# Optimization experiments

Hardware: AMD Instinct MI355X
Metric: run time of the kernel (lower is better)

The kernel has to match this reference:

```python
import jax, jax.numpy as jnp
import numpy as np
from jax import lax

BZ, CAPACITY, SEQ_LEN, IN_VAR, N_EDGES = 64, 134, 288, 16, 96


def setup_inputs() -> dict:
    key = jax.random.key(0)
    ks = jax.random.split(key, 9)
    s_gcn = 1.0 / np.sqrt(SEQ_LEN)
    s_conv = 1.0 / np.sqrt(IN_VAR * 3)
    s_fc = 1.0 / np.sqrt(2 * IN_VAR)
    return {
        "src": jax.random.normal(ks[0], (BZ, CAPACITY, SEQ_LEN, IN_VAR), dtype=jnp.float32),
        "feature_edge_index": jax.random.randint(ks[1], (2, N_EDGES), 0, IN_VAR, dtype=jnp.int32),
        # SAGEConv(seq_len, seq_len): out = lin_l(mean_neighbors) + lin_r(x); lin_l has bias
        "Wl": jax.random.uniform(ks[2], (SEQ_LEN, SEQ_LEN), jnp.float32, -s_gcn, s_gcn),
        "Wr": jax.random.uniform(ks[3], (SEQ_LEN, SEQ_LEN), jnp.float32, -s_gcn, s_gcn),
        "b_gcn": jax.random.uniform(ks[4], (SEQ_LEN,), jnp.float32, -s_gcn, s_gcn),
        "conv1_w": jax.random.uniform(ks[5], (IN_VAR, IN_VAR, 3), jnp.float32, -s_conv, s_conv),
        "conv2_w": jax.random.uniform(ks[6], (IN_VAR, IN_VAR, 5), jnp.float32, -s_conv, s_conv),
        "fc_w": jax.random.uniform(ks[7], (IN_VAR, 2 * IN_VAR), jnp.float32, -s_fc, s_fc),
        "fc_b": jax.random.uniform(ks[8], (IN_VAR,), jnp.float32, -s_fc, s_fc),
    }


def reference(src, feature_edge_index, Wl, Wr, b_gcn, conv1_w, conv2_w, fc_w, fc_b):
    bz, cap, S, F = src.shape  # [bz, capacity, seq_len, in_var]
    B = bz * cap
    # node features for the feature graph: [B, in_var, seq_len]
    x2 = src.transpose(0, 1, 3, 2).reshape(B, F, S)
    e_src, e_dst = feature_edge_index[0], feature_edge_index[1]
    # SAGEConv mean aggregation over shared edge_index, vectorized across B graphs
    gathered = x2[:, e_src, :]                                   # [B, E, S]
    agg = jnp.zeros_like(x2).at[:, e_dst, :].add(gathered)       # [B, F, S]
    deg = jnp.zeros((F,), x2.dtype).at[e_dst].add(1.0)
    mean = agg / jnp.maximum(deg, 1.0)[None, :, None]
    feat = (jnp.einsum('bns,ts->bnt', mean, Wl)
            + jnp.einsum('bns,ts->bnt', x2, Wr) + b_gcn)          # [B, F, S]
    fea_fea = feat.reshape(bz, cap, F, S).transpose(0, 1, 3, 2)   # [bz,cap,S,F]
    # dual temporal Conv1d branches (same padding, no bias) on [B, F, S]
    dn = ('NCH', 'OIH', 'NCH')
    c1 = lax.conv_general_dilated(x2, conv1_w, (1,), [(1, 1)], dimension_numbers=dn)
    c2 = lax.conv_general_dilated(x2, conv2_w, (2,), [(2, 2)][:1] * 1, dimension_numbers=dn) if False else lax.conv_general_dilated(x2, conv2_w, (1,), [(2, 2)], dimension_numbers=dn)
    temporal = (c1 + c2).transpose(0, 2, 1).reshape(bz, cap, S, F)
    com = jnp.concatenate([fea_fea, temporal], axis=-1)           # [bz,cap,S,2F]
    com = jnp.einsum('bcsf,of->bcso', com, fc_w) + fc_b
    # dropout is identity in eval mode
    return src + com
```

## Files before the change

kernel.cpp:

```cpp
#include <hip/hip_runtime.h>
#include <hip/hip_bf16.h>

typedef short short8 __attribute__((ext_vector_type(8)));
typedef float float4v __attribute__((ext_vector_type(4)));
typedef unsigned short ushort4v __attribute__((ext_vector_type(4)));

#define BTOT 8576
#define SEQ 288
#define NF 16
#define SPN 296
#define XTROWS 294
#define XT_USH (XTROWS * 16)
#define XN_USH (16 * SPN)
#define PBN (XT_USH + XN_USH)
#define WCVW 104

__device__ __forceinline__ unsigned short f2b(float f) {
    union { float f; unsigned u; } v; v.f = f;
    unsigned r = v.u + 0x7FFF + ((v.u >> 16) & 1);
    return (unsigned short)(r >> 16);
}
__device__ __forceinline__ float b2f(unsigned short u) {
    union { unsigned u; float f; } v; v.u = ((unsigned)u) << 16; return v.f;
}

__global__ void wcast_kernel(const float* __restrict__ a, const float* __restrict__ b,
                             unsigned short* __restrict__ o) {
    int i = blockIdx.x * 256 + threadIdx.x;
    o[i]         = f2b(a[i]);
    o[82944 + i] = f2b(b[i]);
}

template<int WPRE>
__device__ __forceinline__ short8 ldw(const unsigned short* __restrict__ wb,
                                      const float* __restrict__ wf, int idx) {
    if (WPRE) {
        return *(const short8*)&wb[idx];
    } else {
        const float* p = &wf[idx];
        float4 w0 = *(const float4*)p, w1 = *(const float4*)(p + 4);
        short8 a;
        a[0] = (short)f2b(w0.x); a[1] = (short)f2b(w0.y);
        a[2] = (short)f2b(w0.z); a[3] = (short)f2b(w0.w);
        a[4] = (short)f2b(w1.x); a[5] = (short)f2b(w1.y);
        a[6] = (short)f2b(w1.z); a[7] = (short)f2b(w1.w);
        return a;
    }
}

#define LDB(KK9, B_) do {                                                      \
    const int s0_ = (KK9) * 32;                                                \
    (B_)[0] = *(const short8*)&xsN0[li * SPN + s0_ + 8 * g];                   \
    (B_)[1] = *(const short8*)&xsN1[li * SPN + s0_ + 8 * g];                   \
} while (0)

#define LDA(WT_, WF_, KK9, A_) do {                                            \
    const int s0_ = (KK9) * 32;                                                \
    _Pragma("unroll")                                                          \
    for (int m_ = 0; m_ < 3; ++m_)                                             \
        if (m_ < nt) (A_)[m_] = ldw<WPRE>(WT_, WF_, arow[m_] + s0_ + 8 * g);   \
} while (0)

#define MFK(A_, B_) do {                                                       \
    _Pragma("unroll")                                                          \
    for (int m_ = 0; m_ < 3; ++m_)                                             \
        if (m_ < nt) {                                                         \
            acc[m_][0] = __builtin_amdgcn_mfma_f32_16x16x32_bf16((A_)[m_], (B_)[0], acc[m_][0], 0, 0, 0); \
            acc[m_][1] = __builtin_amdgcn_mfma_f32_16x16x32_bf16((A_)[m_], (B_)[1], acc[m_][1], 0, 0, 0); \
        }                                                                      \
} while (0)

#define GEMM9(WT_, WF_) do {                                                   \
    short8 aC[3], aN[3];                                                       \
    LDA(WT_, WF_, 0, aC);                                                      \
    LDA(WT_, WF_, 1, aN);                                                      \
    _Pragma("unroll")                                                          \
    for (int kk = 0; kk < 9; ++kk) {                                           \
        short8 bb[2];                                                          \
        LDB(kk, bb);                                                           \
        if (kk & 1) { MFK(aN, bb); if (kk < 7) LDA(WT_, WF_, kk + 2, aN); }    \
        else        { MFK(aC, bb); if (kk < 7) LDA(WT_, WF_, kk + 2, aC); }    \
    }                                                                          \
} while (0)

template<int WPRE>
__global__ __launch_bounds__(512, 6) void stconv_mfma(
    const float* __restrict__ src,
    const int*   __restrict__ eidx,
    const float* __restrict__ Wlf,
    const float* __restrict__ Wrf,
    const unsigned short* __restrict__ Wbf,
    const float* __restrict__ bgcn,
    const float* __restrict__ cw1g,
    const float* __restrict__ cw2g,
    const float* __restrict__ fcwg,
    const float* __restrict__ fcbg,
    float*       __restrict__ out)
{
    __shared__ unsigned short pool[2 * PBN];
    __shared__ unsigned short wcv[16 * WCVW];
    __shared__ unsigned short fcwB[16 * 40];
    __shared__ unsigned short MB[16 * 40];
    __shared__ float bg[SEQ];
    __shared__ float Msc[256];
    __shared__ float fcb[16];

    const int tid  = threadIdx.x;
    const int wav  = tid >> 6;
    const int nb   = wav >> 2;
    const int wloc = wav & 3;
    const int lane = tid & 63;
    const int li   = lane & 15;
    const int g    = lane >> 4;
    const int b0   = blockIdx.x * 2;

    unsigned short* xsT = pool + nb * PBN;
    unsigned short* xsN = pool + nb * PBN + XT_USH;
    const float* srcb = src + (size_t)(b0 + nb) * (SEQ * NF);

    if (tid < 256) Msc[tid] = 0.0f;
    for (int i = tid; i < 16 * 40; i += 512) MB[i] = 0;
    for (int i = tid; i < 16 * WCVW; i += 512) wcv[i] = 0;
    if (tid < 192) {
        int nb2 = tid / 96, r2 = tid % 96;
        int r = r2 >> 4, f = r2 & 15;
        int row = (r < 2) ? r : 288 + r;
        pool[nb2 * PBN + row * 16 + f] = 0;
    }
    __syncthreads();

    if (tid < 96) atomicAdd(&Msc[eidx[96 + tid] * 16 + eidx[tid]], 1.0f);
    {
        const int q = tid & 255;
        #pragma unroll
        for (int i = 0; i < 2; ++i) {
            int blk = i * 256 + q;
            if (blk < 288) {
                int s0 = (blk >> 2) * 4, f0 = (blk & 3) * 4;
                ushort4v h[4];
                #pragma unroll
                for (int r = 0; r < 4; ++r) {
                    float4 v = *(const float4*)(srcb + (s0 + r) * 16 + f0);
                    h[r][0] = f2b(v.x); h[r][1] = f2b(v.y);
                    h[r][2] = f2b(v.z); h[r][3] = f2b(v.w);
                    *(ushort4v*)&xsT[(s0 + r + 2) * 16 + f0] = h[r];
                }
                #pragma unroll
                for (int c = 0; c < 4; ++c) {
                    ushort4v w;
                    w[0] = h[0][c]; w[1] = h[1][c]; w[2] = h[2][c]; w[3] = h[3][c];
                    *(ushort4v*)&xsN[(f0 + c) * SPN + s0] = w;
                }
            }
        }
    }
    for (int j = tid; j < 1280; j += 512) {
        int fo = j / 80, rem = j % 80, fi = rem / 5, d = rem % 5;
        float t = cw2g[(fo * 16 + fi) * 5 + d];
        if (d >= 1 && d <= 3) t += cw1g[(fo * 16 + fi) * 3 + (d - 1)];
        wcv[fo * WCVW + d * 16 + fi] = f2b(t);
    }
    if (tid < 512) fcwB[(tid >> 5) * 40 + (tid & 31)] = f2b(fcwg[tid]);
    if (tid < SEQ) bg[tid] = bgcn[tid];
    if (tid < 16) fcb[tid] = fcbg[tid];
    __syncthreads();

    if (tid < 16) {
        float deg = 0.0f;
        #pragma unroll
        for (int f = 0; f < 16; ++f) deg += Msc[tid * 16 + f];
        float inv = 1.0f / fmaxf(deg, 1.0f);
        #pragma unroll
        for (int f = 0; f < 16; ++f) MB[tid * 40 + f] = f2b(Msc[tid * 16 + f] * inv);
    }
    __syncthreads();

    const int t2 = (wav == 0) ? 16 : ((wav == 5) ? 17 : -1);
    const int nt = (t2 >= 0) ? 3 : 2;
    const int tts[3] = {wav, wav + 8, t2};
    const int arow[3] = {(tts[0] * 16 + li) * 288, (tts[1] * 16 + li) * 288,
                         (t2 >= 0) ? ((t2 * 16 + li) * 288) : 0};

    const unsigned short* WblT = Wbf;
    const unsigned short* WbrT = Wbf + 288 * 288;
    const unsigned short* xsN0 = pool + XT_USH;
    const unsigned short* xsN1 = pool + PBN + XT_USH;

    float4v acc[3][2];

    #pragma unroll
    for (int m = 0; m < 3; ++m)
        if (m < nt) {
            #pragma unroll
            for (int r = 0; r < 4; ++r) {
                float bv = bg[tts[m] * 16 + 4 * g + r];
                acc[m][0][r] = bv; acc[m][1][r] = bv;
            }
        }
    GEMM9(WbrT, Wrf);
    __syncthreads();

    {
        short8 bm = *(const short8*)&MB[li * 40 + 8 * g];
        unsigned short* msN = xsN;
        for (int st = wloc; st < 18; st += 4) {
            int s0 = st * 16;
            short8 a = {0, 0, 0, 0, 0, 0, 0, 0};
            if (g < 2) a = *(const short8*)&xsT[(s0 + li + 2) * 16 + 8 * g];
            float4v c = {0.f, 0.f, 0.f, 0.f};
            c = __builtin_amdgcn_mfma_f32_16x16x32_bf16(a, bm, c, 0, 0, 0);
            ushort4v p;
            #pragma unroll
            for (int r = 0; r < 4; ++r) p[r] = f2b(c[r]);
            *(ushort4v*)&msN[li * SPN + s0 + 4 * g] = p;
        }
    }
    __syncthreads();

    GEMM9(WblT, Wlf);

    ushort4v p5o[3][2];
    #pragma unroll
    for (int m = 0; m < 3; ++m)
        if (m < nt) {
            #pragma unroll
            for (int r = 0; r < 4; ++r) {
                p5o[m][0][r] = f2b(acc[m][0][r]);
                p5o[m][1][r] = f2b(acc[m][1][r]);
            }
        }

    ushort4v p6o[5];
    {
        short8 cb0 = *(const short8*)&wcv[li * WCVW + 0  + 8 * g];
        short8 cb1 = *(const short8*)&wcv[li * WCVW + 32 + 8 * g];
        short8 cb2 = *(const short8*)&wcv[li * WCVW + 64 + 8 * g];
        const int fi0   = (g & 1) * 8;
        const int dbase = g >> 1;
        #pragma unroll
        for (int it = 0; it < 5; ++it) {
            int st = wloc + 4 * it;
            if (st < 18) {
                int s0 = st * 16;
                int rbase = (s0 + li + dbase) * 16 + fi0;
                short8 a0 = *(const short8*)&xsT[rbase];
                short8 a1 = *(const short8*)&xsT[rbase + 32];
                short8 a2 = *(const short8*)&xsT[rbase + 64];
                float4v c = {0.f, 0.f, 0.f, 0.f};
                c = __builtin_amdgcn_mfma_f32_16x16x32_bf16(a0, cb0, c, 0, 0, 0);
                c = __builtin_amdgcn_mfma_f32_16x16x32_bf16(a1, cb1, c, 0, 0, 0);
                c = __builtin_amdgcn_mfma_f32_16x16x32_bf16(a2, cb2, c, 0, 0, 0);
                #pragma unroll
                for (int r = 0; r < 4; ++r) p6o[it][r] = f2b(c[r]);
            }
        }
    }

    ushort4v res16[5];
    #pragma unroll
    for (int it = 0; it < 5; ++it) {
        int st = wloc + 4 * it;
        if (st < 18) {
            int s0 = st * 16;
            #pragma unroll
            for (int r = 0; r < 4; ++r)
                res16[it][r] = xsT[(s0 + 4 * g + r + 2) * 16 + li];
        }
    }
    __syncthreads();

    {
        unsigned short* cat0 = pool;
        unsigned short* cat1 = pool + PBN;
        #pragma unroll
        for (int m = 0; m < 3; ++m)
            if (m < nt) {
                #pragma unroll
                for (int r = 0; r < 4; ++r) {
                    int pos = tts[m] * 16 + 4 * g + r;
                    cat0[pos * 32 + li] = p5o[m][0][r];
                    cat1[pos * 32 + li] = p5o[m][1][r];
                }
            }
        unsigned short* catb = pool + nb * PBN;
        #pragma unroll
        for (int it = 0; it < 5; ++it) {
            int st = wloc + 4 * it;
            if (st < 18) {
                int s0 = st * 16;
                #pragma unroll
                for (int r = 0; r < 4; ++r)
                    catb[(s0 + 4 * g + r) * 32 + 16 + li] = p6o[it][r];
            }
        }
    }
    __syncthreads();

    {
        const unsigned short* catb = pool + nb * PBN;
        short8 fb = *(const short8*)&fcwB[li * 40 + 8 * g];
        float* outb = out + (size_t)(b0 + nb) * (SEQ * NF);
        #pragma unroll
        for (int it = 0; it < 5; ++it) {
            int st = wloc + 4 * it;
            if (st < 18) {
                int s0 = st * 16;
                float4v c;
                #pragma unroll
                for (int r = 0; r < 4; ++r) c[r] = b2f(res16[it][r]) + fcb[li];
                short8 a = *(const short8*)&catb[(s0 + li) * 32 + 8 * g];
                c = __builtin_amdgcn_mfma_f32_16x16x32_bf16(a, fb, c, 0, 0, 0);
                #pragma unroll
                for (int r = 0; r < 4; ++r) outb[(s0 + 4 * g + r) * 16 + li] = c[r];
            }
        }
    }
}

extern "C" void kernel_launch(void* const* d_in, const int* in_sizes, int n_in,
                              void* d_out, int out_size, void* d_ws, size_t ws_size,
                              hipStream_t stream)
{
    const float* src  = (const float*)d_in[0];
    const int*   eidx = (const int*)  d_in[1];
    const float* Wl   = (const float*)d_in[2];
    const float* Wr   = (const float*)d_in[3];
    const float* bgcn = (const float*)d_in[4];
    const float* cw1  = (const float*)d_in[5];
    const float* cw2  = (const float*)d_in[6];
    const float* fcw  = (const float*)d_in[7];
    const float* fcb  = (const float*)d_in[8];
    float* out = (float*)d_out;

    const size_t wbytes = (size_t)2 * 288 * 288 * sizeof(unsigned short);
    if (ws_size >= wbytes) {
        wcast_kernel<<<dim3(324), dim3(256), 0, stream>>>(Wl, Wr, (unsigned short*)d_ws);
        stconv_mfma<1><<<dim3(BTOT / 2), dim3(512), 0, stream>>>(
            src, eidx, Wl, Wr, (const unsigned short*)d_ws,
            bgcn, cw1, cw2, fcw, fcb, out);
    } else {
        stconv_mfma<0><<<dim3(BTOT / 2), dim3(512), 0, stream>>>(
            src, eidx, Wl, Wr, nullptr,
            bgcn, cw1, cw2, fcw, fcb, out);
    }
}
```

Baseline: 157.8 us.

## Process one graph per 256-thread block instead of two per 512-thread block

Changes the work split so each block handles a single graph with 4 waves. Each wave now owns 4–5 output row tiles of the 288x288 GEMM instead of 2–3 tiles across two graphs. Per block, weight A-fragments are reused across more M-tiles rather than across two B operands. This halves LDS per block and may allow more resident blocks, but each weight load now feeds only one graph, roughly doubling global and L2 weight traffic per graph.

```diff
diff --git a/kernel.cpp b/kernel.cpp
--- a/kernel.cpp
+++ b/kernel.cpp
@@ -50,33 +50,30 @@
 
 #define LDB(KK9, B_) do {                                                      \
     const int s0_ = (KK9) * 32;                                                \
-    (B_)[0] = *(const short8*)&xsN0[li * SPN + s0_ + 8 * g];                   \
-    (B_)[1] = *(const short8*)&xsN1[li * SPN + s0_ + 8 * g];                   \
+    (B_) = *(const short8*)&xsN[li * SPN + s0_ + 8 * g];                       \
 } while (0)
 
 #define LDA(WT_, WF_, KK9, A_) do {                                            \
     const int s0_ = (KK9) * 32;                                                \
     _Pragma("unroll")                                                          \
-    for (int m_ = 0; m_ < 3; ++m_)                                             \
+    for (int m_ = 0; m_ < 5; ++m_)                                             \
         if (m_ < nt) (A_)[m_] = ldw<WPRE>(WT_, WF_, arow[m_] + s0_ + 8 * g);   \
 } while (0)
 
 #define MFK(A_, B_) do {                                                       \
     _Pragma("unroll")                                                          \
-    for (int m_ = 0; m_ < 3; ++m_)                                             \
-        if (m_ < nt) {                                                         \
-            acc[m_][0] = __builtin_amdgcn_mfma_f32_16x16x32_bf16((A_)[m_], (B_)[0], acc[m_][0], 0, 0, 0); \
-            acc[m_][1] = __builtin_amdgcn_mfma_f32_16x16x32_bf16((A_)[m_], (B_)[1], acc[m_][1], 0, 0, 0); \
-        }                                                                      \
+    for (int m_ = 0; m_ < 5; ++m_)                                             \
+        if (m_ < nt)                                                           \
+            acc[m_] = __builtin_amdgcn_mfma_f32_16x16x32_bf16((A_)[m_], (B_), acc[m_], 0, 0, 0); \
 } while (0)
 
 #define GEMM9(WT_, WF_) do {                                                   \
-    short8 aC[3], aN[3];                                                       \
+    short8 aC[5], aN[5];                                                       \
     LDA(WT_, WF_, 0, aC);                                                      \
     LDA(WT_, WF_, 1, aN);                                                      \
     _Pragma("unroll")                                                          \
     for (int kk = 0; kk < 9; ++kk) {                                           \
-        short8 bb[2];                                                          \
+        short8 bb;                                                             \
         LDB(kk, bb);                                                           \
         if (kk & 1) { MFK(aN, bb); if (kk < 7) LDA(WT_, WF_, kk + 2, aN); }    \
         else        { MFK(aC, bb); if (kk < 7) LDA(WT_, WF_, kk + 2, aC); }    \
@@ -84,7 +81,7 @@
 } while (0)
 
 template<int WPRE>
-__global__ __launch_bounds__(512, 6) void stconv_mfma(
+__global__ __launch_bounds__(256, 6) void stconv_mfma(
     const float* __restrict__ src,
     const int*   __restrict__ eidx,
     const float* __restrict__ Wlf,
@@ -97,7 +94,7 @@
     const float* __restrict__ fcbg,
     float*       __restrict__ out)
 {
-    __shared__ unsigned short pool[2 * PBN];
+    __shared__ unsigned short pool[PBN];
     __shared__ unsigned short wcv[16 * WCVW];
     __shared__ unsigned short fcwB[16 * 40];
     __shared__ unsigned short MB[16 * 40];
@@ -107,34 +104,30 @@
 
     const int tid  = threadIdx.x;
     const int wav  = tid >> 6;
-    const int nb   = wav >> 2;
-    const int wloc = wav & 3;
     const int lane = tid & 63;
     const int li   = lane & 15;
     const int g    = lane >> 4;
-    const int b0   = blockIdx.x * 2;
-
-    unsigned short* xsT = pool + nb * PBN;
-    unsigned short* xsN = pool + nb * PBN + XT_USH;
-    const float* srcb = src + (size_t)(b0 + nb) * (SEQ * NF);
-
-    if (tid < 256) Msc[tid] = 0.0f;
-    for (int i = tid; i < 16 * 40; i += 512) MB[i] = 0;
-    for (int i = tid; i < 16 * WCVW; i += 512) wcv[i] = 0;
-    if (tid < 192) {
-        int nb2 = tid / 96, r2 = tid % 96;
-        int r = r2 >> 4, f = r2 & 15;
+    const int b    = blockIdx.x;
+
+    unsigned short* xsT = pool;
+    unsigned short* xsN = pool + XT_USH;
+    const float* srcb = src + (size_t)b * (SEQ * NF);
+
+    Msc[tid] = 0.0f;
+    for (int i = tid; i < 16 * 40; i += 256) MB[i] = 0;
+    for (int i = tid; i < 16 * WCVW; i += 256) wcv[i] = 0;
+    if (tid < 96) {
+        int r = tid >> 4, f = tid & 15;
         int row = (r < 2) ? r : 288 + r;
-        pool[nb2 * PBN + row * 16 + f] = 0;
+        xsT[row * 16 + f] = 0;
     }
     __syncthreads();
 
     if (tid < 96) atomicAdd(&Msc[eidx[96 + tid] * 16 + eidx[tid]], 1.0f);
     {
-        const int q = tid & 255;
         #pragma unroll
         for (int i = 0; i < 2; ++i) {
-            int blk = i * 256 + q;
+            int blk = i * 256 + tid;
             if (blk < 288) {
                 int s0 = (blk >> 2) * 4, f0 = (blk & 3) * 4;
                 ushort4v h[4];
@@ -154,14 +147,14 @@
             }
         }
     }
-    for (int j = tid; j < 1280; j += 512) {
+    for (int j = tid; j < 1280; j += 256) {
         int fo = j / 80, rem = j % 80, fi = rem / 5, d = rem % 5;
         float t = cw2g[(fo * 16 + fi) * 5 + d];
         if (d >= 1 && d <= 3) t += cw1g[(fo * 16 + fi) * 3 + (d - 1)];
         wcv[fo * WCVW + d * 16 + fi] = f2b(t);
     }
-    if (tid < 512) fcwB[(tid >> 5) * 40 + (tid & 31)] = f2b(fcwg[tid]);
-    if (tid < SEQ) bg[tid] = bgcn[tid];
+    for (int j = tid; j < 512; j += 256) fcwB[(j >> 5) * 40 + (j & 31)] = f2b(fcwg[j]);
+    for (int i = tid; i < SEQ; i += 256) bg[i] = bgcn[i];
     if (tid < 16) fcb[tid] = fcbg[tid];
     __syncthreads();
 
@@ -175,27 +168,24 @@
     }
     __syncthreads();
 
-    const int t2 = (wav == 0) ? 16 : ((wav == 5) ? 17 : -1);
-    const int nt = (t2 >= 0) ? 3 : 2;
-    const int tts[3] = {wav, wav + 8, t2};
-    const int arow[3] = {(tts[0] * 16 + li) * 288, (tts[1] * 16 + li) * 288,
-                         (t2 >= 0) ? ((t2 * 16 + li) * 288) : 0};
+    const int t4 = (wav < 2) ? (16 + wav) : -1;
+    const int nt = (t4 >= 0) ? 5 : 4;
+    const int tts[5] = {wav, wav + 4, wav + 8, wav + 12, t4};
+    const int arow[5] = {(tts[0] * 16 + li) * 288, (tts[1] * 16 + li) * 288,
+                         (tts[2] * 16 + li) * 288, (tts[3] * 16 + li) * 288,
+                         (t4 >= 0) ? ((t4 * 16 + li) * 288) : 0};
 
     const unsigned short* WblT = Wbf;
     const unsigned short* WbrT = Wbf + 288 * 288;
-    const unsigned short* xsN0 = pool + XT_USH;
-    const unsigned short* xsN1 = pool + PBN + XT_USH;
-
-    float4v acc[3][2];
+
+    float4v acc[5];
 
     #pragma unroll
-    for (int m = 0; m < 3; ++m)
+    for (int m = 0; m < 5; ++m)
         if (m < nt) {
             #pragma unroll
-            for (int r = 0; r < 4; ++r) {
-                float bv = bg[tts[m] * 16 + 4 * g + r];
-                acc[m][0][r] = bv; acc[m][1][r] = bv;
-            }
+            for (int r = 0; r < 4; ++r)
+                acc[m][r] = bg[tts[m] * 16 + 4 * g + r];
         }
     GEMM9(WbrT, Wrf);
     __syncthreads();
@@ -203,7 +193,7 @@
     {
         short8 bm = *(const short8*)&MB[li * 40 + 8 * g];
         unsigned short* msN = xsN;
-        for (int st = wloc; st < 18; st += 4) {
+        for (int st = wav; st < 18; st += 4) {
             int s0 = st * 16;
             short8 a = {0, 0, 0, 0, 0, 0, 0, 0};
             if (g < 2) a = *(const short8*)&xsT[(s0 + li + 2) * 16 + 8 * g];
@@ -219,15 +209,13 @@
 
     GEMM9(WblT, Wlf);
 
-    ushort4v p5o[3][2];
+    ushort4v p5o[5];
     #pragma unroll
-    for (int m = 0; m < 3; ++m)
+    for (int m = 0; m < 5; ++m)
         if (m < nt) {
             #pragma unroll
-            for (int r = 0; r < 4; ++r) {
-                p5o[m][0][r] = f2b(acc[m][0][r]);
-                p5o[m][1][r] = f2b(acc[m][1][r]);
-            }
+            for (int r = 0; r < 4; ++r)
+                p5o[m][r] = f2b(acc[m][r]);
         }
 
     ushort4v p6o[5];
@@ -239,7 +227,7 @@
         const int dbase = g >> 1;
         #pragma unroll
         for (int it = 0; it < 5; ++it) {
-            int st = wloc + 4 * it;
+            int st = wav + 4 * it;
             if (st < 18) {
                 int s0 = st * 16;
                 int rbase = (s0 + li + dbase) * 16 + fi0;
@@ -259,7 +247,7 @@
     ushort4v res16[5];
     #pragma unroll
     for (int it = 0; it < 5; ++it) {
-        int st = wloc + 4 * it;
+        int st = wav + 4 * it;
         if (st < 18) {
             int s0 = st * 16;
             #pragma unroll
@@ -270,45 +258,42 @@
     __syncthreads();
 
     {
-        unsigned short* cat0 = pool;
-        unsigned short* cat1 = pool + PBN;
-        #pragma unroll
-        for (int m = 0; m < 3; ++m)
+        unsigned short* cat = pool;
+        #pragma unroll
+        for (int m = 0; m < 5; ++m)
             if (m < nt) {
                 #pragma unroll
                 for (int r = 0; r < 4; ++r) {
                     int pos = tts[m] * 16 + 4 * g + r;
-                    cat0[pos * 32 + li] = p5o[m][0][r];
-                    cat1[pos * 32 + li] = p5o[m][1][r];
+                    cat[pos * 32 + li] = p5o[m][r];
                 }
             }
-        unsigned short* catb = pool + nb * PBN;
         #pragma unroll
         for (int it = 0; it < 5; ++it) {
-            int st = wloc + 4 * it;
+            int st = wav + 4 * it;
             if (st < 18) {
                 int s0 = st * 16;
                 #pragma unroll
                 for (int r = 0; r < 4; ++r)
-                    catb[(s0 + 4 * g + r) * 32 + 16 + li] = p6o[it][r];
-            }
-        }
-    }
-    __syncthreads();
-
-    {
-        const unsigned short* catb = pool + nb * PBN;
+                    cat[(s0 + 4 * g + r) * 32 + 16 + li] = p6o[it][r];
+            }
+        }
+    }
+    __syncthreads();
+
+    {
+        const unsigned short* cat = pool;
         short8 fb = *(const short8*)&fcwB[li * 40 + 8 * g];
-        float* outb = out + (size_t)(b0 + nb) * (SEQ * NF);
+        float* outb = out + (size_t)b * (SEQ * NF);
         #pragma unroll
         for (int it = 0; it < 5; ++it) {
-            int st = wloc + 4 * it;
+            int st = wav + 4 * it;
             if (st < 18) {
                 int s0 = st * 16;
                 float4v c;
                 #pragma unroll
                 for (int r = 0; r < 4; ++r) c[r] = b2f(res16[it][r]) + fcb[li];
-                short8 a = *(const short8*)&catb[(s0 + li) * 32 + 8 * g];
+                short8 a = *(const short8*)&cat[(s0 + li) * 32 + 8 * g];
                 c = __builtin_amdgcn_mfma_f32_16x16x32_bf16(a, fb, c, 0, 0, 0);
                 #pragma unroll
                 for (int r = 0; r < 4; ++r) outb[(s0 + 4 * g + r) * 16 + li] = c[r];
@@ -335,11 +320,11 @@
     const size_t wbytes = (size_t)2 * 288 * 288 * sizeof(unsigned short);
     if (ws_size >= wbytes) {
         wcast_kernel<<<dim3(324), dim3(256), 0, stream>>>(Wl, Wr, (unsigned short*)d_ws);
-        stconv_mfma<1><<<dim3(BTOT / 2), dim3(512), 0, stream>>>(
+        stconv_mfma<1><<<dim3(BTOT), dim3(256), 0, stream>>>(
             src, eidx, Wl, Wr, (const unsigned short*)d_ws,
             bgcn, cw1, cw2, fcw, fcb, out);
     } else {
-        stconv_mfma<0><<<dim3(BTOT / 2), dim3(512), 0, stream>>>(
+        stconv_mfma<0><<<dim3(BTOT), dim3(256), 0, stream>>>(
             src, eidx, Wl, Wr, nullptr,
             bgcn, cw1, cw2, fcw, fcb, out);
     }
```

Measured after the change: 350.3 us. +122.0%, slower.

## Process three graphs per block to reuse each weight fragment across more MFMAs

Applied to the files above, without the earlier changes.

Each block now handles three batch graphs instead of two, so every bf16 Wl/Wr A-fragment loaded in the SAGE GEMM feeds three MFMA columns rather than two, cutting weight traffic per graph. The elementwise, conv and FC stages are redistributed over all 8 waves across the three graphs, and the launch bound drops from 6 to 4 blocks per SM to leave room for more accumulators. The trade is more registers and LDS per block, which lowers occupancy. Because 8576 is not divisible by 3, the final block clamps to the last graph and recomputes it, writing the same values twice.

```diff
diff --git a/kernel.cpp b/kernel.cpp
--- a/kernel.cpp
+++ b/kernel.cpp
@@ -8,6 +8,7 @@
 #define BTOT 8576
 #define SEQ 288
 #define NF 16
+#define NB 3
 #define SPN 296
 #define XTROWS 294
 #define XT_USH (XTROWS * 16)
@@ -52,6 +53,7 @@
     const int s0_ = (KK9) * 32;                                                \
     (B_)[0] = *(const short8*)&xsN0[li * SPN + s0_ + 8 * g];                   \
     (B_)[1] = *(const short8*)&xsN1[li * SPN + s0_ + 8 * g];                   \
+    (B_)[2] = *(const short8*)&xsN2[li * SPN + s0_ + 8 * g];                   \
 } while (0)
 
 #define LDA(WT_, WF_, KK9, A_) do {                                            \
@@ -67,6 +69,7 @@
         if (m_ < nt) {                                                         \
             acc[m_][0] = __builtin_amdgcn_mfma_f32_16x16x32_bf16((A_)[m_], (B_)[0], acc[m_][0], 0, 0, 0); \
             acc[m_][1] = __builtin_amdgcn_mfma_f32_16x16x32_bf16((A_)[m_], (B_)[1], acc[m_][1], 0, 0, 0); \
+            acc[m_][2] = __builtin_amdgcn_mfma_f32_16x16x32_bf16((A_)[m_], (B_)[2], acc[m_][2], 0, 0, 0); \
         }                                                                      \
 } while (0)
 
@@ -76,7 +79,7 @@
     LDA(WT_, WF_, 1, aN);                                                      \
     _Pragma("unroll")                                                          \
     for (int kk = 0; kk < 9; ++kk) {                                           \
-        short8 bb[2];                                                          \
+        short8 bb[NB];                                                         \
         LDB(kk, bb);                                                           \
         if (kk & 1) { MFK(aN, bb); if (kk < 7) LDA(WT_, WF_, kk + 2, aN); }    \
         else        { MFK(aC, bb); if (kk < 7) LDA(WT_, WF_, kk + 2, aC); }    \
@@ -84,7 +87,7 @@
 } while (0)
 
 template<int WPRE>
-__global__ __launch_bounds__(512, 6) void stconv_mfma(
+__global__ __launch_bounds__(512, 4) void stconv_mfma(
     const float* __restrict__ src,
     const int*   __restrict__ eidx,
     const float* __restrict__ Wlf,
@@ -97,7 +100,7 @@
     const float* __restrict__ fcbg,
     float*       __restrict__ out)
 {
-    __shared__ unsigned short pool[2 * PBN];
+    __shared__ unsigned short pool[NB * PBN];
     __shared__ unsigned short wcv[16 * WCVW];
     __shared__ unsigned short fcwB[16 * 40];
     __shared__ unsigned short MB[16 * 40];
@@ -107,21 +110,19 @@
 
     const int tid  = threadIdx.x;
     const int wav  = tid >> 6;
-    const int nb   = wav >> 2;
-    const int wloc = wav & 3;
     const int lane = tid & 63;
     const int li   = lane & 15;
     const int g    = lane >> 4;
-    const int b0   = blockIdx.x * 2;
-
-    unsigned short* xsT = pool + nb * PBN;
-    unsigned short* xsN = pool + nb * PBN + XT_USH;
-    const float* srcb = src + (size_t)(b0 + nb) * (SEQ * NF);
+    const int b0   = blockIdx.x * NB;
+
+    int bid[NB];
+    #pragma unroll
+    for (int n = 0; n < NB; ++n) bid[n] = (b0 + n < BTOT) ? (b0 + n) : (BTOT - 1);
 
     if (tid < 256) Msc[tid] = 0.0f;
     for (int i = tid; i < 16 * 40; i += 512) MB[i] = 0;
     for (int i = tid; i < 16 * WCVW; i += 512) wcv[i] = 0;
-    if (tid < 192) {
+    if (tid < 288) {
         int nb2 = tid / 96, r2 = tid % 96;
         int r = r2 >> 4, f = r2 & 15;
         int row = (r < 2) ? r : 288 + r;
@@ -131,11 +132,14 @@
 
     if (tid < 96) atomicAdd(&Msc[eidx[96 + tid] * 16 + eidx[tid]], 1.0f);
     {
-        const int q = tid & 255;
         #pragma unroll
         for (int i = 0; i < 2; ++i) {
-            int blk = i * 256 + q;
-            if (blk < 288) {
+            int u = i * 512 + tid;
+            if (u < NB * 288) {
+                int nbu = u / 288, blk = u % 288;
+                const float* srcb = src + (size_t)bid[0] * 0  + (size_t)((nbu == 0) ? bid[0] : (nbu == 1) ? bid[1] : bid[2]) * (SEQ * NF);
+                unsigned short* xsTu = pool + nbu * PBN;
+                unsigned short* xsNu = pool + nbu * PBN + XT_USH;
                 int s0 = (blk >> 2) * 4, f0 = (blk & 3) * 4;
                 ushort4v h[4];
                 #pragma unroll
@@ -143,13 +147,13 @@
                     float4 v = *(const float4*)(srcb + (s0 + r) * 16 + f0);
                     h[r][0] = f2b(v.x); h[r][1] = f2b(v.y);
                     h[r][2] = f2b(v.z); h[r][3] = f2b(v.w);
-                    *(ushort4v*)&xsT[(s0 + r + 2) * 16 + f0] = h[r];
+                    *(ushort4v*)&xsTu[(s0 + r + 2) * 16 + f0] = h[r];
                 }
                 #pragma unroll
                 for (int c = 0; c < 4; ++c) {
                     ushort4v w;
                     w[0] = h[0][c]; w[1] = h[1][c]; w[2] = h[2][c]; w[3] = h[3][c];
-                    *(ushort4v*)&xsN[(f0 + c) * SPN + s0] = w;
+                    *(ushort4v*)&xsNu[(f0 + c) * SPN + s0] = w;
                 }
             }
         }
@@ -183,10 +187,11 @@
 
     const unsigned short* WblT = Wbf;
     const unsigned short* WbrT = Wbf + 288 * 288;
-    const unsigned short* xsN0 = pool + XT_USH;
-    const unsigned short* xsN1 = pool + PBN + XT_USH;
-
-    float4v acc[3][2];
+    const unsigned short* xsN0 = pool + 0 * PBN + XT_USH;
+    const unsigned short* xsN1 = pool + 1 * PBN + XT_USH;
+    const unsigned short* xsN2 = pool + 2 * PBN + XT_USH;
+
+    float4v acc[3][NB];
 
     #pragma unroll
     for (int m = 0; m < 3; ++m)
@@ -194,7 +199,8 @@
             #pragma unroll
             for (int r = 0; r < 4; ++r) {
                 float bv = bg[tts[m] * 16 + 4 * g + r];
-                acc[m][0][r] = bv; acc[m][1][r] = bv;
+                #pragma unroll
+                for (int n = 0; n < NB; ++n) acc[m][n][r] = bv;
             }
         }
     GEMM9(WbrT, Wrf);
@@ -202,35 +208,42 @@
 
     {
         short8 bm = *(const short8*)&MB[li * 40 + 8 * g];
-        unsigned short* msN = xsN;
-        for (int st = wloc; st < 18; st += 4) {
-            int s0 = st * 16;
-            short8 a = {0, 0, 0, 0, 0, 0, 0, 0};
-            if (g < 2) a = *(const short8*)&xsT[(s0 + li + 2) * 16 + 8 * g];
-            float4v c = {0.f, 0.f, 0.f, 0.f};
-            c = __builtin_amdgcn_mfma_f32_16x16x32_bf16(a, bm, c, 0, 0, 0);
-            ushort4v p;
-            #pragma unroll
-            for (int r = 0; r < 4; ++r) p[r] = f2b(c[r]);
-            *(ushort4v*)&msN[li * SPN + s0 + 4 * g] = p;
+        #pragma unroll
+        for (int it = 0; it < 7; ++it) {
+            int u = wav + 8 * it;
+            if (u < NB * 18) {
+                int nbu = u / 18, st = u % 18;
+                unsigned short* xsTu = pool + nbu * PBN;
+                unsigned short* msNu = pool + nbu * PBN + XT_USH;
+                int s0 = st * 16;
+                short8 a = {0, 0, 0, 0, 0, 0, 0, 0};
+                if (g < 2) a = *(const short8*)&xsTu[(s0 + li + 2) * 16 + 8 * g];
+                float4v c = {0.f, 0.f, 0.f, 0.f};
+                c = __builtin_amdgcn_mfma_f32_16x16x32_bf16(a, bm, c, 0, 0, 0);
+                ushort4v p;
+                #pragma unroll
+                for (int r = 0; r < 4; ++r) p[r] = f2b(c[r]);
+                *(ushort4v*)&msNu[li * SPN + s0 + 4 * g] = p;
+            }
         }
     }
     __syncthreads();
 
     GEMM9(WblT, Wlf);
 
-    ushort4v p5o[3][2];
+    ushort4v p5o[3][NB];
     #pragma unroll
     for (int m = 0; m < 3; ++m)
         if (m < nt) {
             #pragma unroll
-            for (int r = 0; r < 4; ++r) {
-                p5o[m][0][r] = f2b(acc[m][0][r]);
-                p5o[m][1][r] = f2b(acc[m][1][r]);
-            }
-        }
-
-    ushort4v p6o[5];
+            for (int n = 0; n < NB; ++n) {
+                #pragma unroll
+                for (int r = 0; r < 4; ++r)
+                    p5o[m][n][r] = f2b(acc[m][n][r]);
+            }
+        }
+
+    ushort4v p6o[7];
     {
         short8 cb0 = *(const short8*)&wcv[li * WCVW + 0  + 8 * g];
         short8 cb1 = *(const short8*)&wcv[li * WCVW + 32 + 8 * g];
@@ -238,14 +251,16 @@
         const int fi0   = (g & 1) * 8;
         const int dbase = g >> 1;
         #pragma unroll
-        for (int it = 0; it < 5; ++it) {
-            int st = wloc + 4 * it;
-            if (st < 18) {
+        for (int it = 0; it < 7; ++it) {
+            int u = wav + 8 * it;
+            if (u < NB * 18) {
+                int nbu = u / 18, st = u % 18;
+                const unsigned short* xsTu = pool + nbu * PBN;
                 int s0 = st * 16;
                 int rbase = (s0 + li + dbase) * 16 + fi0;
-                short8 a0 = *(const short8*)&xsT[rbase];
-                short8 a1 = *(const short8*)&xsT[rbase + 32];
-                short8 a2 = *(const short8*)&xsT[rbase + 64];
+                short8 a0 = *(const short8*)&xsTu[rbase];
+                short8 a1 = *(const short8*)&xsTu[rbase + 32];
+                short8 a2 = *(const short8*)&xsTu[rbase + 64];
                 float4v c = {0.f, 0.f, 0.f, 0.f};
                 c = __builtin_amdgcn_mfma_f32_16x16x32_bf16(a0, cb0, c, 0, 0, 0);
                 c = __builtin_amdgcn_mfma_f32_16x16x32_bf16(a1, cb1, c, 0, 0, 0);
@@ -256,59 +271,64 @@
         }
     }
 
-    ushort4v res16[5];
+    ushort4v res16[7];
     #pragma unroll
-    for (int it = 0; it < 5; ++it) {
-        int st = wloc + 4 * it;
-        if (st < 18) {
+    for (int it = 0; it < 7; ++it) {
+        int u = wav + 8 * it;
+        if (u < NB * 18) {
+            int nbu = u / 18, st = u % 18;
+            const unsigned short* xsTu = pool + nbu * PBN;
             int s0 = st * 16;
             #pragma unroll
             for (int r = 0; r < 4; ++r)
-                res16[it][r] = xsT[(s0 + 4 * g + r + 2) * 16 + li];
-        }
-    }
-    __syncthreads();
-
-    {
-        unsigned short* cat0 = pool;
-        unsigned short* cat1 = pool + PBN;
+                res16[it][r] = xsTu[(s0 + 4 * g + r + 2) * 16 + li];
+        }
+    }
+    __syncthreads();
+
+    {
         #pragma unroll
         for (int m = 0; m < 3; ++m)
             if (m < nt) {
                 #pragma unroll
-                for (int r = 0; r < 4; ++r) {
-                    int pos = tts[m] * 16 + 4 * g + r;
-                    cat0[pos * 32 + li] = p5o[m][0][r];
-                    cat1[pos * 32 + li] = p5o[m][1][r];
+                for (int n = 0; n < NB; ++n) {
+                    unsigned short* catn = pool + n * PBN;
+                    #pragma unroll
+                    for (int r = 0; r < 4; ++r) {
+                        int pos = tts[m] * 16 + 4 * g + r;
+                        catn[pos * 32 + li] = p5o[m][n][r];
+                    }
                 }
             }
-        unsigned short* catb = pool + nb * PBN;
-        #pragma unroll
-        for (int it = 0; it < 5; ++it) {
-            int st = wloc + 4 * it;
-            if (st < 18) {
+        #pragma unroll
+        for (int it = 0; it < 7; ++it) {
+            int u = wav + 8 * it;
+            if (u < NB * 18) {
+                int nbu = u / 18, st = u % 18;
+                unsigned short* catn = pool + nbu * PBN;
                 int s0 = st * 16;
                 #pragma unroll
                 for (int r = 0; r < 4; ++r)
-                    catb[(s0 + 4 * g + r) * 32 + 16 + li] = p6o[it][r];
-            }
-        }
-    }
-    __syncthreads();
-
-    {
-        const unsigned short* catb = pool + nb * PBN;
+                    catn[(s0 + 4 * g + r) * 32 + 16 + li] = p6o[it][r];
+            }
+        }
+    }
+    __syncthreads();
+
+    {
         short8 fb = *(const short8*)&fcwB[li * 40 + 8 * g];
-        float* outb = out + (size_t)(b0 + nb) * (SEQ * NF);
-        #pragma unroll
-        for (int it = 0; it < 5; ++it) {
-            int st = wloc + 4 * it;
-            if (st < 18) {
+        #pragma unroll
+        for (int it = 0; it < 7; ++it) {
+            int u = wav + 8 * it;
+            if (u < NB * 18) {
+                int nbu = u / 18, st = u % 18;
+                const unsigned short* catn = pool + nbu * PBN;
+                float* outb = out + (size_t)bid[0] * 0 + (size_t)((nbu == 0) ? bid[0] : (nbu == 1) ? bid[1] : bid[2]) * (SEQ * NF);
                 int s0 = st * 16;
                 float4v c;
                 #pragma unroll
                 for (int r = 0; r < 4; ++r) c[r] = b2f(res16[it][r]) + fcb[li];
-                short8 a = *(const short8*)&catb[(s0 + li) * 32 + 8 * g];
+                short8 a = *(const short8*)&catn[(s0 + li) * 32 + 8 * g];
                 c = __builtin_amdgcn_mfma_f32_16x16x32_bf16(a, fb, c, 0, 0, 0);
                 #pragma unroll
                 for (int r = 0; r < 4; ++r) outb[(s0 + 4 * g + r) * 16 + li] = c[r];
@@ -332,14 +352,15 @@
     const float* fcb  = (const float*)d_in[8];
     float* out = (float*)d_out;
 
+    const int grid = (BTOT + NB - 1) / NB;
     const size_t wbytes = (size_t)2 * 288 * 288 * sizeof(unsigned short);
     if (ws_size >= wbytes) {
         wcast_kernel<<<dim3(324), dim3(256), 0, stream>>>(Wl, Wr, (unsigned short*)d_ws);
-        stconv_mfma<1><<<dim3(BTOT / 2), dim3(512), 0, stream>>>(
+        stconv_mfma<1><<<dim3(grid), dim3(512), 0, stream>>>(
             src, eidx, Wl, Wr, (const unsigned short*)d_ws,
             bgcn, cw1, cw2, fcw, fcb, out);
     } else {
-        stconv_mfma<0><<<dim3(BTOT / 2), dim3(512), 0, stream>>>(
+        stconv_mfma<0><<<dim3(grid), dim3(512), 0, stream>>>(
             src, eidx, Wl, Wr, nullptr,
             bgcn, cw1, cw2, fcw, fcb, out);
     }
```

Result: faster. 143.8 us (-8.9%).
